# Kernel tuning notes

Measured on AMD Instinct MI355X. Metric: run time of the kernel, lower is better.

## Reference

```python
import jax, jax.numpy as jnp
import numpy as np

EMBED = 512
HEADS = 8
HEAD_DIM = EMBED // HEADS


def setup_inputs() -> dict:
    key = jax.random.key(0)
    ks = jax.random.split(key, 9)
    N, L = 4, 2048
    values = jax.random.normal(ks[0], (N, L, EMBED), dtype=jnp.float32)
    keys = jax.random.normal(ks[1], (N, L, EMBED), dtype=jnp.float32)
    query = jax.random.normal(ks[2], (N, L, EMBED), dtype=jnp.float32)
    mask = jax.random.randint(ks[3], (N, 1, 1, L), 0, 2, dtype=jnp.int32)
    s_h = 1.0 / np.sqrt(HEAD_DIM).astype(np.float32)
    s_e = 1.0 / np.sqrt(EMBED).astype(np.float32)
    Wv = jax.random.normal(ks[4], (HEAD_DIM, HEAD_DIM), dtype=jnp.float32) * s_h
    Wk = jax.random.normal(ks[5], (HEAD_DIM, HEAD_DIM), dtype=jnp.float32) * s_h
    Wq = jax.random.normal(ks[6], (HEAD_DIM, HEAD_DIM), dtype=jnp.float32) * s_h
    Wo = jax.random.normal(ks[7], (EMBED, EMBED), dtype=jnp.float32) * s_e
    bo = jnp.zeros((EMBED,), dtype=jnp.float32)
    return {"values": values, "keys": keys, "query": query, "mask": mask,
            "Wv": Wv, "Wk": Wk, "Wq": Wq, "Wo": Wo, "bo": bo}


def reference(values, keys, query, mask, Wv, Wk, Wq, Wo, bo):
    N, Lq, E = query.shape
    D = Wv.shape[0]
    H = E // D
    Lk = keys.shape[1]
    # split heads: [N, L, H, D]
    v = values.reshape(N, values.shape[1], H, D)
    k = keys.reshape(N, Lk, H, D)
    q = query.reshape(N, Lq, H, D)
    # per-head linear projections (nn.Linear: x @ W^T, no bias)
    v = jnp.einsum("nlhd,ed->nlhe", v, Wv)
    k = jnp.einsum("nlhd,ed->nlhe", k, Wk)
    q = jnp.einsum("nlhd,ed->nlhe", q, Wq)
    # energy: [N, H, Lq, Lk]
    energy = jnp.einsum("nqhd,nkhd->nhqk", q, k)
    energy = jnp.where(mask == 0, jnp.float32(-1e20), energy)
    # NOTE: original scales by sqrt(embed_size), not sqrt(head_dim)
    attn = jax.nn.softmax(energy / jnp.sqrt(jnp.float32(E)), axis=3)
    out = jnp.einsum("nhqk,nkhd->nqhd", attn, v).reshape(N, Lq, E)
    return out @ Wo.T + bo
```

## Files before the change

### kernel.cpp

```cpp
#include <hip/hip_runtime.h>

#define LSEQ 2048
#define EMB  512
#define NH   8
#define HD   64
#define NBATCH 4
#define QSCALE (0.044194173824159216f * 1.4426950408889634f)

using short8  = __attribute__((ext_vector_type(8))) short;
using short4v = __attribute__((ext_vector_type(4))) short;
using f32x4   = __attribute__((ext_vector_type(4))) float;

__device__ __forceinline__ short bf16r(float f) {
  union { float f; unsigned u; } x; x.f = f;
  unsigned r = x.u + 0x7FFFu + ((x.u >> 16) & 1u);
  return (short)(r >> 16);
}

__device__ __forceinline__ float exp2v(float x) {
  float r;
  asm("v_exp_f32 %0, %1" : "=v"(r) : "v"(x));
  return r;
}

__device__ __forceinline__ unsigned cvtpk(float lo, float hi) {
  unsigned r;
  asm("v_cvt_pk_bf16_f32 %0, %1, %2" : "=v"(r) : "v"(lo), "v"(hi));
  return r;
}

__device__ __forceinline__ void stage16(const void* g, void* l) {
  __builtin_amdgcn_global_load_lds(
      (const __attribute__((address_space(1))) unsigned int*)g,
      (__attribute__((address_space(3))) unsigned int*)l, 16, 0, 0);
}

__device__ __forceinline__ short8 cvt8(const float* __restrict__ p) {
  float4 a = ((const float4*)p)[0];
  float4 b = ((const float4*)p)[1];
  short8 r;
  r[0]=bf16r(a.x); r[1]=bf16r(a.y); r[2]=bf16r(a.z); r[3]=bf16r(a.w);
  r[4]=bf16r(b.x); r[5]=bf16r(b.y); r[6]=bf16r(b.z); r[7]=bf16r(b.w);
  return r;
}

__device__ __forceinline__ short8 ld8(const short* __restrict__ p) {
  return *(const short8*)p;
}

__global__ __launch_bounds__(256) void prep_kernel(
    const int* __restrict__ mask, float* __restrict__ fbias,
    int* __restrict__ kidx, int* __restrict__ meta,
    const float* __restrict__ Wq, const float* __restrict__ Wk,
    const float* __restrict__ Wv, short* __restrict__ Wqb,
    short* __restrict__ Wkb, short* __restrict__ Wvb) {
  __shared__ int ssum[256];
  int b = blockIdx.x;
  int tid = threadIdx.x;
  if (b < 4) {
    int n = b;
    int base = n * LSEQ;
    int loc[8], c = 0;
#pragma unroll
    for (int j = 0; j < 8; j++) { loc[j] = mask[base + tid * 8 + j] != 0; c += loc[j]; }
    ssum[tid] = c;
    __syncthreads();
    for (int off = 1; off < 256; off <<= 1) {
      int v = (tid >= off) ? ssum[tid - off] : 0;
      __syncthreads();
      ssum[tid] += v;
      __syncthreads();
    }
    int total = ssum[255];
    int excl = ssum[tid] - c;
    int qz = (total == 0);
#pragma unroll
    for (int j = 0; j < 8; j++) {
      int i = tid * 8 + j;
      kidx[base + i] = qz ? i : 0;
      fbias[base + i] = (qz || i < total) ? 0.f : -1e30f;
    }
    __syncthreads();
    if (!qz) {
      int pos = excl;
#pragma unroll
      for (int j = 0; j < 8; j++)
        if (loc[j]) { kidx[base + pos] = tid * 8 + j; pos++; }
    }
    if (tid == 0) {
      meta[n] = qz ? (LSEQ / 64) : ((total + 63) >> 6);
      meta[4 + n] = qz;
    }
  } else {
    int t = (b - 4) >> 2;
    int i = ((b - 4) & 3) * 256 + tid;
    const float* W = (t == 0) ? Wq : (t == 1) ? Wk : Wv;
    short* O = (t == 0) ? Wqb : (t == 1) ? Wkb : Wvb;
    float sc = (t == 0) ? QSCALE : 1.f;
    float4 v = ((const float4*)W)[i];
    short4v r;
    r[0]=bf16r(v.x*sc); r[1]=bf16r(v.y*sc); r[2]=bf16r(v.z*sc); r[3]=bf16r(v.w*sc);
    ((short4v*)O)[i] = r;
  }
}

__global__ __launch_bounds__(256) void proj_kernel(
    const float* __restrict__ query, const float* __restrict__ keys,
    const float* __restrict__ values,
    const short* __restrict__ Wqb, const short* __restrict__ Wkb,
    const short* __restrict__ Wvb, const int* __restrict__ kidx,
    const int* __restrict__ meta,
    short* __restrict__ Qp, short* __restrict__ Kp, short* __restrict__ Vt) {
  __shared__ short tile[64][72];
  int t = blockIdx.y;
  const float* x = (t == 0) ? query : (t == 1) ? keys : values;
  const short* W = (t == 0) ? Wqb   : (t == 1) ? Wkb  : Wvb;
  int idx = blockIdx.x;
  int lt = idx & 31, h = (idx >> 5) & 7, n = idx >> 8;
  int tid = threadIdx.x, lane = tid & 63, w = tid >> 6;
  int row16 = lane & 15, g = lane >> 4;
  int lbase = lt * 64 + w * 16;

  int zq = 0;
  const float* xr;
  int lrow = lbase + row16;
  if (t == 0) {
    zq = meta[4 + n];
    xr = x + ((size_t)(n * LSEQ + lrow)) * EMB + h * HD + g * 8;
  } else {
    if (lbase >= ((meta[n] + 1) & ~1) * 64) return;
    int gidx = kidx[n * LSEQ + lrow];
    xr = x + ((size_t)(n * LSEQ + gidx)) * EMB + h * HD + g * 8;
  }
  short8 a0 = cvt8(xr);
  short8 a1 = cvt8(xr + 32);

  f32x4 acc[4];
#pragma unroll
  for (int et = 0; et < 4; et++) acc[et] = (f32x4){0.f, 0.f, 0.f, 0.f};
#pragma unroll
  for (int et = 0; et < 4; et++) {
    const short* wr = W + (size_t)(et * 16 + row16) * HD + g * 8;
    short8 b0 = ld8(wr);
    short8 b1 = ld8(wr + 32);
    acc[et] = __builtin_amdgcn_mfma_f32_16x16x32_bf16(a0, b0, acc[et], 0, 0, 0);
    acc[et] = __builtin_amdgcn_mfma_f32_16x16x32_bf16(a1, b1, acc[et], 0, 0, 0);
  }
  if (zq) {
#pragma unroll
    for (int et = 0; et < 4; et++) acc[et] = (f32x4){0.f, 0.f, 0.f, 0.f};
  }

  if (t == 2) {
#pragma unroll
    for (int et = 0; et < 4; et++)
#pragma unroll
      for (int r = 0; r < 4; r++)
        tile[et * 16 + row16][w * 16 + g * 4 + r] = bf16r(acc[et][r]);
  } else {
#pragma unroll
    for (int et = 0; et < 4; et++)
#pragma unroll
      for (int r = 0; r < 4; r++)
        tile[w * 16 + g * 4 + r][et * 16 + row16] = bf16r(acc[et][r]);
  }
  __syncthreads();

  size_t nh = (size_t)(n * NH + h);
#pragma unroll
  for (int i = tid; i < 512; i += 256) {
    int rr = i >> 3, cc = i & 7;
    short8 v = *(const short8*)&tile[rr][cc * 8];
    if (t == 2)
      *(short8*)(Vt + (nh * HD + rr) * LSEQ + lt * 64 + cc * 8) = v;
    else {
      short* O = (t == 0) ? Qp : Kp;
      *(short8*)(O + (nh * LSEQ + lt * 64 + rr) * HD + cc * 8) = v;
    }
  }
}

__global__ __launch_bounds__(512, 1) void attn_kernel(
    const short* __restrict__ Qp, const short* __restrict__ Kp,
    const short* __restrict__ Vt, const float* __restrict__ fbias,
    const int* __restrict__ meta, short* __restrict__ aout,
    const float* __restrict__ Wo, short* __restrict__ Wob) {
  __shared__ __align__(16) char smem[98304];

  int idx = blockIdx.x;
  int tid = threadIdx.x;
  if (idx >= NBATCH * NH * (LSEQ / 256)) {
    int i = (idx - NBATCH * NH * (LSEQ / 256)) * 512 + tid;
    float4 v = ((const float4*)Wo)[i];
    short4v r;
    r[0]=bf16r(v.x); r[1]=bf16r(v.y); r[2]=bf16r(v.z); r[3]=bf16r(v.w);
    ((short4v*)Wob)[i] = r;
    return;
  }
  int h = idx & 7;
  int qt = (idx >> 3) & 7;
  int n = idx >> 6;
  int lane = tid & 63, w = tid >> 6;
  int q0 = lane & 15, g = lane >> 4;
  int xr = q0 & 7;
  int nkt = (meta[n] + 1) >> 1;

  size_t nh = (size_t)(n * NH + h);
  const short* Qb = Qp + (nh * LSEQ + qt * 256 + w * 32) * HD;
  short8 bq00 = ld8(Qb + q0 * HD + g * 8);
  short8 bq01 = ld8(Qb + q0 * HD + 32 + g * 8);
  short8 bq10 = ld8(Qb + (16 + q0) * HD + g * 8);
  short8 bq11 = ld8(Qb + (16 + q0) * HD + 32 + g * 8);

  f32x4 acc0[4], acc1[4];
#pragma unroll
  for (int dt = 0; dt < 4; dt++) {
    acc0[dt] = (f32x4){0.f, 0.f, 0.f, 0.f};
    acc1[dt] = (f32x4){0.f, 0.f, 0.f, 0.f};
  }
  float l0 = 0.f, l1 = 0.f;

  const char* Ksrc = (const char*)(Kp + nh * (size_t)LSEQ * HD);
  const char* Vsrc = (const char*)(Vt + nh * (size_t)HD * LSEQ);
  const float* fb  = fbias + n * LSEQ + g * 4;

  int ksoff[2], vsoff[2], ldo[2];
#pragma unroll
  for (int j = 0; j < 2; j++) {
    int c = j * 512 + w * 64 + lane;
    int rK = c >> 3, cwK = (c & 7) ^ (rK & 7);
    ksoff[j] = rK * 128 + cwK * 16;
    int rV = c >> 4, cwV = c & 15;
    int sub = (cwV & 7) ^ (rV & 7);
    vsoff[j] = rV * (LSEQ * 2) + ((cwV & 8) + sub) * 16;
    ldo[j] = (j * 512 + w * 64) * 16;
  }

  int kfragb = q0 * 128 + ((g ^ xr) << 4);
  int vfragb = q0 * 256 + ((g ^ xr) << 4);
  int pbase = 65536 + w * 4096 + q0 * 128;
  char* pw_[4];
#pragma unroll
  for (int ks = 0; ks < 4; ks++)
    pw_[ks] = smem + pbase + ((ks * 32 + g * 8) ^ (xr << 4));
  const char* pr0 = smem + pbase + ((g * 16) ^ (xr << 4));
  const char* pr1 = smem + pbase + ((64 + g * 16) ^ (xr << 4));

#pragma unroll
  for (int j = 0; j < 2; j++) stage16(Ksrc + ksoff[j], smem + ldo[j]);
#pragma unroll
  for (int j = 0; j < 2; j++) stage16(Vsrc + vsoff[j], smem + 32768 + ldo[j]);
  __syncthreads();

  for (int kt = 0; kt < nkt; kt++) {
    int buf = kt & 1;
    if (kt < nkt - 1) {
      int bo = (buf ^ 1) * 16384;
      const char* Kn = Ksrc + (size_t)(kt + 1) * (128 * 128);
      const char* Vn = Vsrc + (size_t)(kt + 1) * 256;
#pragma unroll
      for (int j = 0; j < 2; j++) stage16(Kn + ksoff[j], smem + bo + ldo[j]);
#pragma unroll
      for (int j = 0; j < 2; j++) stage16(Vn + vsoff[j], smem + 32768 + bo + ldo[j]);
    }

#pragma unroll
    for (int h2 = 0; h2 < 2; h2++) {
      f32x4 fbv[4];
#pragma unroll
      for (int ks = 0; ks < 4; ks++)
        fbv[ks] = *(const f32x4*)(fb + kt * 128 + h2 * 64 + ks * 16);

      int kb_l = buf * 16384 + h2 * 8192 + kfragb;
      f32x4 s0[4], s1[4];
      __builtin_amdgcn_s_setprio(1);
#pragma unroll
      for (int ks = 0; ks < 4; ks++) {
        short8 k0 = *(const short8*)(smem + (kb_l + ks * 2048));
        short8 k1 = *(const short8*)(smem + ((kb_l + ks * 2048) ^ 64));
        f32x4 t0 = __builtin_amdgcn_mfma_f32_16x16x32_bf16(k0, bq00, fbv[ks], 0, 0, 0);
        s0[ks]   = __builtin_amdgcn_mfma_f32_16x16x32_bf16(k1, bq01, t0, 0, 0, 0);
        f32x4 t1 = __builtin_amdgcn_mfma_f32_16x16x32_bf16(k0, bq10, fbv[ks], 0, 0, 0);
        s1[ks]   = __builtin_amdgcn_mfma_f32_16x16x32_bf16(k1, bq11, t1, 0, 0, 0);
      }
      __builtin_amdgcn_s_setprio(0);

      float ps0 = 0.f, ps1 = 0.f;
#pragma unroll
      for (int ks = 0; ks < 4; ks++) {
        float p0 = exp2v(s0[ks][0] - 32.f), p1 = exp2v(s0[ks][1] - 32.f);
        float p2 = exp2v(s0[ks][2] - 32.f), p3 = exp2v(s0[ks][3] - 32.f);
        ps0 += (p0 + p1) + (p2 + p3);
        *(int2*)pw_[ks] = make_int2((int)cvtpk(p0, p1), (int)cvtpk(p2, p3));
        float q1 = exp2v(s1[ks][0] - 32.f), q2 = exp2v(s1[ks][1] - 32.f);
        float q3 = exp2v(s1[ks][2] - 32.f), q4 = exp2v(s1[ks][3] - 32.f);
        ps1 += (q1 + q2) + (q3 + q4);
        *(int2*)(pw_[ks] + 2048) = make_int2((int)cvtpk(q1, q2), (int)cvtpk(q3, q4));
      }
      l0 += ps0; l1 += ps1;

      asm volatile("s_waitcnt lgkmcnt(0)" ::: "memory");

      short8 ap00 = *(const short8*)pr0;
      short8 ap01 = *(const short8*)pr1;
      short8 ap10 = *(const short8*)(pr0 + 2048);
      short8 ap11 = *(const short8*)(pr1 + 2048);
      int vb_l = 32768 + buf * 16384 + vfragb + h2 * 128;
      __builtin_amdgcn_s_setprio(1);
#pragma unroll
      for (int dt = 0; dt < 4; dt++) {
        short8 v0 = *(const short8*)(smem + (vb_l + dt * 4096));
        short8 v1 = *(const short8*)(smem + ((vb_l + dt * 4096) ^ 64));
        acc0[dt] = __builtin_amdgcn_mfma_f32_16x16x32_bf16(ap00, v0, acc0[dt], 0, 0, 0);
        acc0[dt] = __builtin_amdgcn_mfma_f32_16x16x32_bf16(ap01, v1, acc0[dt], 0, 0, 0);
        acc1[dt] = __builtin_amdgcn_mfma_f32_16x16x32_bf16(ap10, v0, acc1[dt], 0, 0, 0);
        acc1[dt] = __builtin_amdgcn_mfma_f32_16x16x32_bf16(ap11, v1, acc1[dt], 0, 0, 0);
      }
      __builtin_amdgcn_s_setprio(0);
    }

    __syncthreads();
  }

  l0 += __shfl_xor(l0, 16);  l0 += __shfl_xor(l0, 32);
  l1 += __shfl_xor(l1, 16);  l1 += __shfl_xor(l1, 32);
  float li0 = l0 > 0.f ? 1.f / l0 : 0.f;
  float li1 = l1 > 0.f ? 1.f / l1 : 0.f;
  int lb = lane & 48;
  float w0[4], w1[4];
#pragma unroll
  for (int r = 0; r < 4; r++) {
    w0[r] = __shfl(li0, lb + g * 4 + r);
    w1[r] = __shfl(li1, lb + g * 4 + r);
  }
  int qrow = qt * 256 + w * 32;
#pragma unroll
  for (int r = 0; r < 4; r++) {
    size_t o0 = ((size_t)(n * LSEQ + qrow + g * 4 + r)) * EMB + h * HD;
    size_t o1 = ((size_t)(n * LSEQ + qrow + 16 + g * 4 + r)) * EMB + h * HD;
#pragma unroll
    for (int dt = 0; dt < 4; dt++) {
      aout[o0 + dt * 16 + q0] = bf16r(acc0[dt][r] * w0[r]);
      aout[o1 + dt * 16 + q0] = bf16r(acc1[dt][r] * w1[r]);
    }
  }
}

__global__ __launch_bounds__(256) void outproj_kernel(
    const short* __restrict__ aout, const short* __restrict__ Wob,
    const float* __restrict__ bo, float* __restrict__ out) {
  int mt = blockIdx.x, nt = blockIdx.y;
  int tid = threadIdx.x, lane = tid & 63, w = tid >> 6;
  int row16 = lane & 15, g = lane >> 4;
  int mrow = mt * 256 + w * 64;

  f32x4 acc[4][4];
#pragma unroll
  for (int hh = 0; hh < 4; hh++)
#pragma unroll
    for (int et = 0; et < 4; et++) acc[hh][et] = (f32x4){0.f, 0.f, 0.f, 0.f};

  for (int kc = 0; kc < 16; kc++) {
    short8 a[4];
#pragma unroll
    for (int hh = 0; hh < 4; hh++)
      a[hh] = ld8(aout + (size_t)(mrow + hh * 16 + row16) * EMB + kc * 32 + g * 8);
#pragma unroll
    for (int et = 0; et < 4; et++) {
      short8 bw = ld8(Wob + (size_t)(nt * 64 + et * 16 + row16) * EMB + kc * 32 + g * 8);
#pragma unroll
      for (int hh = 0; hh < 4; hh++)
        acc[hh][et] = __builtin_amdgcn_mfma_f32_16x16x32_bf16(a[hh], bw, acc[hh][et], 0, 0, 0);
    }
  }
#pragma unroll
  for (int et = 0; et < 4; et++) {
    int e = nt * 64 + et * 16 + row16;
    float bias = bo[e];
#pragma unroll
    for (int hh = 0; hh < 4; hh++)
#pragma unroll
      for (int r = 0; r < 4; r++)
        out[(size_t)(mrow + hh * 16 + g * 4 + r) * EMB + e] = acc[hh][et][r] + bias;
  }
}

extern "C" void kernel_launch(void* const* d_in, const int* in_sizes, int n_in,
                              void* d_out, int out_size, void* d_ws, size_t ws_size,
                              hipStream_t stream) {
  const float* values = (const float*)d_in[0];
  const float* keys   = (const float*)d_in[1];
  const float* query  = (const float*)d_in[2];
  const int*   mask   = (const int*)d_in[3];
  const float* Wv     = (const float*)d_in[4];
  const float* Wk     = (const float*)d_in[5];
  const float* Wq     = (const float*)d_in[6];
  const float* Wo     = (const float*)d_in[7];
  const float* bo     = (const float*)d_in[8];
  float* out = (float*)d_out;

  short* Qp = (short*)d_out;
  short* Kp = (short*)((char*)d_out + (8u << 20));
  char* ws = (char*)d_ws;
  short* Vt    = (short*)(ws);
  short* aout  = (short*)(ws + (8u << 20));
  short* Wob   = (short*)(ws + (16u << 20));
  float* fbias = (float*)(ws + (16u << 20) + (512u << 10));
  int*   kidx  = (int*)  (ws + (16u << 20) + (544u << 10));
  int*   meta  = (int*)  (ws + (16u << 20) + (576u << 10));
  short* Wqb   = (short*)(ws + (16u << 20) + (577u << 10));
  short* Wkb   = (short*)(ws + (16u << 20) + (585u << 10));
  short* Wvb   = (short*)(ws + (16u << 20) + (593u << 10));

  prep_kernel<<<16, 256, 0, stream>>>(mask, fbias, kidx, meta,
                                      Wq, Wk, Wv, Wqb, Wkb, Wvb);
  proj_kernel<<<dim3(NBATCH * NH * (LSEQ / 64), 3), 256, 0, stream>>>(
      query, keys, values, Wqb, Wkb, Wvb, kidx, meta, Qp, Kp, Vt);
  attn_kernel<<<NBATCH * NH * (LSEQ / 256) + 128, 512, 0, stream>>>(
      Qp, Kp, Vt, fbias, meta, aout, Wo, Wob);
  outproj_kernel<<<dim3((NBATCH * LSEQ) / 256, EMB / 64), 256, 0, stream>>>(
      aout, Wob, bo, out);
}
```

Measured before the change: 84.00 us.

## Fuse four kernels into two cooperative launches with grid-wide syncs

Merges prep and projection into one cooperative kernel, and attention and output projection into another, with grid.sync between the phases instead of separate launches. The Wo bf16 conversion moves into the first fused kernel, and the output projection is remapped onto the 256 attention blocks, using 128 of them with 8 waves each. This is meant to cut launch overheads and inter-kernel gaps. The cost is grid-sync overhead, reduced parallelism in the outproj phase (128 blocks instead of 256), and reliance on all 1536 or 256 blocks being co-resident, with a fallback to separate launches if the cooperative launch fails.

After: 299.7 us. 257% more time.

```diff
diff --git a/kernel.cpp b/kernel.cpp
--- a/kernel.cpp
+++ b/kernel.cpp
@@ -1,4 +1,7 @@
 #include <hip/hip_runtime.h>
+#include <hip/hip_cooperative_groups.h>
+
+namespace cg = cooperative_groups;
 
 #define LSEQ 2048
 #define EMB  512
@@ -48,87 +51,69 @@
   return *(const short8*)p;
 }
 
-__global__ __launch_bounds__(256) void prep_kernel(
-    const int* __restrict__ mask, float* __restrict__ fbias,
-    int* __restrict__ kidx, int* __restrict__ meta,
-    const float* __restrict__ Wq, const float* __restrict__ Wk,
-    const float* __restrict__ Wv, short* __restrict__ Wqb,
-    short* __restrict__ Wkb, short* __restrict__ Wvb) {
-  __shared__ int ssum[256];
-  int b = blockIdx.x;
-  int tid = threadIdx.x;
-  if (b < 4) {
-    int n = b;
-    int base = n * LSEQ;
-    int loc[8], c = 0;
-#pragma unroll
-    for (int j = 0; j < 8; j++) { loc[j] = mask[base + tid * 8 + j] != 0; c += loc[j]; }
-    ssum[tid] = c;
+
+__device__ __forceinline__ void compact_phase(int n, const int* __restrict__ mask,
+                                              float* __restrict__ fbias,
+                                              int* __restrict__ kidx,
+                                              int* __restrict__ meta, int* ssum,
+                                              int tid) {
+  int base = n * LSEQ;
+  int loc[8], c = 0;
+#pragma unroll
+  for (int j = 0; j < 8; j++) { loc[j] = mask[base + tid * 8 + j] != 0; c += loc[j]; }
+  ssum[tid] = c;
+  __syncthreads();
+  for (int off = 1; off < 256; off <<= 1) {
+    int v = (tid >= off) ? ssum[tid - off] : 0;
     __syncthreads();
-    for (int off = 1; off < 256; off <<= 1) {
-      int v = (tid >= off) ? ssum[tid - off] : 0;
-      __syncthreads();
-      ssum[tid] += v;
-      __syncthreads();
-    }
-    int total = ssum[255];
-    int excl = ssum[tid] - c;
-    int qz = (total == 0);
-#pragma unroll
-    for (int j = 0; j < 8; j++) {
-      int i = tid * 8 + j;
-      kidx[base + i] = qz ? i : 0;
-      fbias[base + i] = (qz || i < total) ? 0.f : -1e30f;
-    }
+    ssum[tid] += v;
     __syncthreads();
-    if (!qz) {
-      int pos = excl;
-#pragma unroll
-      for (int j = 0; j < 8; j++)
-        if (loc[j]) { kidx[base + pos] = tid * 8 + j; pos++; }
-    }
-    if (tid == 0) {
-      meta[n] = qz ? (LSEQ / 64) : ((total + 63) >> 6);
-      meta[4 + n] = qz;
-    }
-  } else {
-    int t = (b - 4) >> 2;
-    int i = ((b - 4) & 3) * 256 + tid;
-    const float* W = (t == 0) ? Wq : (t == 1) ? Wk : Wv;
-    short* O = (t == 0) ? Wqb : (t == 1) ? Wkb : Wvb;
-    float sc = (t == 0) ? QSCALE : 1.f;
-    float4 v = ((const float4*)W)[i];
-    short4v r;
-    r[0]=bf16r(v.x*sc); r[1]=bf16r(v.y*sc); r[2]=bf16r(v.z*sc); r[3]=bf16r(v.w*sc);
-    ((short4v*)O)[i] = r;
-  }
-}
-
-__global__ __launch_bounds__(256) void proj_kernel(
+  }
+  int total = ssum[255];
+  int excl = ssum[tid] - c;
+  int qz = (total == 0);
+#pragma unroll
+  for (int j = 0; j < 8; j++) {
+    int i = tid * 8 + j;
+    kidx[base + i] = qz ? i : 0;
+    fbias[base + i] = (qz || i < total) ? 0.f : -1e30f;
+  }
+  __syncthreads();
+  if (!qz) {
+    int pos = excl;
+#pragma unroll
+    for (int j = 0; j < 8; j++)
+      if (loc[j]) { kidx[base + pos] = tid * 8 + j; pos++; }
+  }
+  if (tid == 0) {
+    meta[n] = qz ? (LSEQ / 64) : ((total + 63) >> 6);
+    meta[4 + n] = qz;
+  }
+}
+
+__device__ __forceinline__ void proj_unit(
+    int u, int tid, short (*tile)[72],
     const float* __restrict__ query, const float* __restrict__ keys,
     const float* __restrict__ values,
     const short* __restrict__ Wqb, const short* __restrict__ Wkb,
     const short* __restrict__ Wvb, const int* __restrict__ kidx,
     const int* __restrict__ meta,
     short* __restrict__ Qp, short* __restrict__ Kp, short* __restrict__ Vt) {
-  __shared__ short tile[64][72];
-  int t = blockIdx.y;
+  int t = u >> 10, pidx = u & 1023;
+  int lt = pidx & 31, h = (pidx >> 5) & 7, n = pidx >> 8;
+  if (t != 0 && lt * 64 >= ((meta[n] + 1) & ~1) * 64) return;
   const float* x = (t == 0) ? query : (t == 1) ? keys : values;
   const short* W = (t == 0) ? Wqb   : (t == 1) ? Wkb  : Wvb;
-  int idx = blockIdx.x;
-  int lt = idx & 31, h = (idx >> 5) & 7, n = idx >> 8;
-  int tid = threadIdx.x, lane = tid & 63, w = tid >> 6;
+  int lane = tid & 63, w = tid >> 6;
   int row16 = lane & 15, g = lane >> 4;
   int lbase = lt * 64 + w * 16;
-
+  int lrow = lbase + row16;
   int zq = 0;
   const float* xr;
-  int lrow = lbase + row16;
   if (t == 0) {
     zq = meta[4 + n];
     xr = x + ((size_t)(n * LSEQ + lrow)) * EMB + h * HD + g * 8;
   } else {
-    if (lbase >= ((meta[n] + 1) & ~1) * 64) return;
     int gidx = kidx[n * LSEQ + lrow];
     xr = x + ((size_t)(n * LSEQ + gidx)) * EMB + h * HD + g * 8;
   }
@@ -167,7 +152,6 @@
   __syncthreads();
 
   size_t nh = (size_t)(n * NH + h);
-#pragma unroll
   for (int i = tid; i < 512; i += 256) {
     int rr = i >> 3, cc = i & 7;
     short8 v = *(const short8*)&tile[rr][cc * 8];
@@ -180,23 +164,11 @@
   }
 }
 
-__global__ __launch_bounds__(512, 1) void attn_kernel(
+__device__ __forceinline__ void attn_block(
+    int idx, int tid, char* smem,
     const short* __restrict__ Qp, const short* __restrict__ Kp,
     const short* __restrict__ Vt, const float* __restrict__ fbias,
-    const int* __restrict__ meta, short* __restrict__ aout,
-    const float* __restrict__ Wo, short* __restrict__ Wob) {
-  __shared__ __align__(16) char smem[98304];
-
-  int idx = blockIdx.x;
-  int tid = threadIdx.x;
-  if (idx >= NBATCH * NH * (LSEQ / 256)) {
-    int i = (idx - NBATCH * NH * (LSEQ / 256)) * 512 + tid;
-    float4 v = ((const float4*)Wo)[i];
-    short4v r;
-    r[0]=bf16r(v.x); r[1]=bf16r(v.y); r[2]=bf16r(v.z); r[3]=bf16r(v.w);
-    ((short4v*)Wob)[i] = r;
-    return;
-  }
+    const int* __restrict__ meta, short* __restrict__ aout) {
   int h = idx & 7;
   int qt = (idx >> 3) & 7;
   int n = idx >> 6;
@@ -346,43 +318,170 @@
   }
 }
 
+__device__ __forceinline__ void outproj_wave(
+    int mrow, int nt, int lane, const short* __restrict__ aout,
+    const short* __restrict__ Wob, const float* __restrict__ bo,
+    float* __restrict__ out) {
+  int row16 = lane & 15, g = lane >> 4;
+  f32x4 acc[4][4];
+#pragma unroll
+  for (int hh = 0; hh < 4; hh++)
+#pragma unroll
+    for (int et = 0; et < 4; et++) acc[hh][et] = (f32x4){0.f, 0.f, 0.f, 0.f};
+
+  for (int kc = 0; kc < 16; kc++) {
+    short8 a[4];
+#pragma unroll
+    for (int hh = 0; hh < 4; hh++)
+      a[hh] = ld8(aout + (size_t)(mrow + hh * 16 + row16) * EMB + kc * 32 + g * 8);
+#pragma unroll
+    for (int et = 0; et < 4; et++) {
+      short8 bw = ld8(Wob + (size_t)(nt * 64 + et * 16 + row16) * EMB + kc * 32 + g * 8);
+#pragma unroll
+      for (int hh = 0; hh < 4; hh++)
+        acc[hh][et] = __builtin_amdgcn_mfma_f32_16x16x32_bf16(a[hh], bw, acc[hh][et], 0, 0, 0);
+    }
+  }
+#pragma unroll
+  for (int et = 0; et < 4; et++) {
+    int e = nt * 64 + et * 16 + row16;
+    float bias = bo[e];
+#pragma unroll
+    for (int hh = 0; hh < 4; hh++)
+#pragma unroll
+      for (int r = 0; r < 4; r++)
+        out[(size_t)(mrow + hh * 16 + g * 4 + r) * EMB + e] = acc[hh][et][r] + bias;
+  }
+}
+
+__global__ __launch_bounds__(256, 6) void fusedA(
+    const int* __restrict__ mask, float* __restrict__ fbias,
+    int* __restrict__ kidx, int* __restrict__ meta,
+    const float* __restrict__ Wq, const float* __restrict__ Wk,
+    const float* __restrict__ Wv, const float* __restrict__ Wo,
+    short* __restrict__ Wqb, short* __restrict__ Wkb, short* __restrict__ Wvb,
+    short* __restrict__ Wob,
+    const float* __restrict__ query, const float* __restrict__ keys,
+    const float* __restrict__ values,
+    short* __restrict__ Qp, short* __restrict__ Kp, short* __restrict__ Vt) {
+  __shared__ __align__(16) char smA[9216];
+  int b = blockIdx.x, tid = threadIdx.x;
+
+  if (b < 4) {
+    compact_phase(b, mask, fbias, kidx, meta, (int*)smA, tid);
+  } else if (b < 16) {
+    int t = (b - 4) >> 2;
+    int i = ((b - 4) & 3) * 256 + tid;
+    const float* W = (t == 0) ? Wq : (t == 1) ? Wk : Wv;
+    short* O = (t == 0) ? Wqb : (t == 1) ? Wkb : Wvb;
+    float sc = (t == 0) ? QSCALE : 1.f;
+    float4 v = ((const float4*)W)[i];
+    short4v r;
+    r[0]=bf16r(v.x*sc); r[1]=bf16r(v.y*sc); r[2]=bf16r(v.z*sc); r[3]=bf16r(v.w*sc);
+    ((short4v*)O)[i] = r;
+  } else if (b < 272) {
+    int i = (b - 16) * 256 + tid;
+    float4 v = ((const float4*)Wo)[i];
+    short4v r;
+    r[0]=bf16r(v.x); r[1]=bf16r(v.y); r[2]=bf16r(v.z); r[3]=bf16r(v.w);
+    ((short4v*)Wob)[i] = r;
+  }
+  cg::this_grid().sync();
+
+  short (*tile)[72] = (short(*)[72])smA;
+#pragma unroll
+  for (int it = 0; it < 2; it++) {
+    int u = b + it * 1536;
+    proj_unit(u, tid, tile, query, keys, values, Wqb, Wkb, Wvb, kidx, meta,
+              Qp, Kp, Vt);
+    __syncthreads();
+  }
+}
+
+__global__ __launch_bounds__(512, 1) void fusedB(
+    const short* __restrict__ Qp, const short* __restrict__ Kp,
+    const short* __restrict__ Vt, const float* __restrict__ fbias,
+    const int* __restrict__ meta, short* __restrict__ aout,
+    const short* __restrict__ Wob, const float* __restrict__ bo,
+    float* __restrict__ out) {
+  __shared__ __align__(16) char smem[98304];
+  int b = blockIdx.x, tid = threadIdx.x;
+
+  attn_block(b, tid, smem, Qp, Kp, Vt, fbias, meta, aout);
+  cg::this_grid().sync();
+
+  if (b < 128) {
+    int lane = tid & 63, w8 = tid >> 6;
+    int mt = b >> 2, ntp = b & 3;
+    int mrow = mt * 256 + (w8 & 3) * 64;
+    int nt = ntp * 2 + (w8 >> 2);
+    outproj_wave(mrow, nt, lane, aout, Wob, bo, out);
+  }
+}
+
+
+__global__ __launch_bounds__(256) void prep_kernel(
+    const int* __restrict__ mask, float* __restrict__ fbias,
+    int* __restrict__ kidx, int* __restrict__ meta,
+    const float* __restrict__ Wq, const float* __restrict__ Wk,
+    const float* __restrict__ Wv, short* __restrict__ Wqb,
+    short* __restrict__ Wkb, short* __restrict__ Wvb) {
+  __shared__ int ssum[256];
+  int b = blockIdx.x;
+  int tid = threadIdx.x;
+  if (b < 4) {
+    compact_phase(b, mask, fbias, kidx, meta, ssum, tid);
+  } else {
+    int t = (b - 4) >> 2;
+    int i = ((b - 4) & 3) * 256 + tid;
+    const float* W = (t == 0) ? Wq : (t == 1) ? Wk : Wv;
+    short* O = (t == 0) ? Wqb : (t == 1) ? Wkb : Wvb;
+    float sc = (t == 0) ? QSCALE : 1.f;
+    float4 v = ((const float4*)W)[i];
+    short4v r;
+    r[0]=bf16r(v.x*sc); r[1]=bf16r(v.y*sc); r[2]=bf16r(v.z*sc); r[3]=bf16r(v.w*sc);
+    ((short4v*)O)[i] = r;
+  }
+}
+
+__global__ __launch_bounds__(256) void proj_kernel(
+    const float* __restrict__ query, const float* __restrict__ keys,
+    const float* __restrict__ values,
+    const short* __restrict__ Wqb, const short* __restrict__ Wkb,
+    const short* __restrict__ Wvb, const int* __restrict__ kidx,
+    const int* __restrict__ meta,
+    short* __restrict__ Qp, short* __restrict__ Kp, short* __restrict__ Vt) {
+  __shared__ short tile[64][72];
+  int u = blockIdx.y * 1024 + blockIdx.x;
+  proj_unit(u, threadIdx.x, tile, query, keys, values, Wqb, Wkb, Wvb,
+            kidx, meta, Qp, Kp, Vt);
+}
+
+__global__ __launch_bounds__(512, 1) void attn_kernel(
+    const short* __restrict__ Qp, const short* __restrict__ Kp,
+    const short* __restrict__ Vt, const float* __restrict__ fbias,
+    const int* __restrict__ meta, short* __restrict__ aout,
+    const float* __restrict__ Wo, short* __restrict__ Wob) {
+  __shared__ __align__(16) char smem[98304];
+  int idx = blockIdx.x;
+  int tid = threadIdx.x;
+  if (idx >= NBATCH * NH * (LSEQ / 256)) {
+    int i = (idx - NBATCH * NH * (LSEQ / 256)) * 512 + tid;
+    float4 v = ((const float4*)Wo)[i];
+    short4v r;
+    r[0]=bf16r(v.x); r[1]=bf16r(v.y); r[2]=bf16r(v.z); r[3]=bf16r(v.w);
+    ((short4v*)Wob)[i] = r;
+    return;
+  }
+  attn_block(idx, tid, smem, Qp, Kp, Vt, fbias, meta, aout);
+}
+
 __global__ __launch_bounds__(256) void outproj_kernel(
     const short* __restrict__ aout, const short* __restrict__ Wob,
     const float* __restrict__ bo, float* __restrict__ out) {
-  int mt = blockIdx.x, nt = blockIdx.y;
-  int tid = threadIdx.x, lane = tid & 63, w = tid >> 6;
-  int row16 = lane & 15, g = lane >> 4;
-  int mrow = mt * 256 + w * 64;
-
-  f32x4 acc[4][4];
-#pragma unroll
-  for (int hh = 0; hh < 4; hh++)
-#pragma unroll
-    for (int et = 0; et < 4; et++) acc[hh][et] = (f32x4){0.f, 0.f, 0.f, 0.f};
-
-  for (int kc = 0; kc < 16; kc++) {
-    short8 a[4];
-#pragma unroll
-    for (int hh = 0; hh < 4; hh++)
-      a[hh] = ld8(aout + (size_t)(mrow + hh * 16 + row16) * EMB + kc * 32 + g * 8);
-#pragma unroll
-    for (int et = 0; et < 4; et++) {
-      short8 bw = ld8(Wob + (size_t)(nt * 64 + et * 16 + row16) * EMB + kc * 32 + g * 8);
-#pragma unroll
-      for (int hh = 0; hh < 4; hh++)
-        acc[hh][et] = __builtin_amdgcn_mfma_f32_16x16x32_bf16(a[hh], bw, acc[hh][et], 0, 0, 0);
-    }
-  }
-#pragma unroll
-  for (int et = 0; et < 4; et++) {
-    int e = nt * 64 + et * 16 + row16;
-    float bias = bo[e];
-#pragma unroll
-    for (int hh = 0; hh < 4; hh++)
-#pragma unroll
-      for (int r = 0; r < 4; r++)
-        out[(size_t)(mrow + hh * 16 + g * 4 + r) * EMB + e] = acc[hh][et][r] + bias;
-  }
+  int lane = threadIdx.x & 63, w = threadIdx.x >> 6;
+  int mrow = blockIdx.x * 256 + w * 64;
+  outproj_wave(mrow, blockIdx.y, lane, aout, Wob, bo, out);
 }
 
 extern "C" void kernel_launch(void* const* d_in, const int* in_sizes, int n_in,
@@ -412,12 +511,37 @@
   short* Wkb   = (short*)(ws + (16u << 20) + (585u << 10));
   short* Wvb   = (short*)(ws + (16u << 20) + (593u << 10));
 
-  prep_kernel<<<16, 256, 0, stream>>>(mask, fbias, kidx, meta,
-                                      Wq, Wk, Wv, Wqb, Wkb, Wvb);
-  proj_kernel<<<dim3(NBATCH * NH * (LSEQ / 64), 3), 256, 0, stream>>>(
-      query, keys, values, Wqb, Wkb, Wvb, kidx, meta, Qp, Kp, Vt);
-  attn_kernel<<<NBATCH * NH * (LSEQ / 256) + 128, 512, 0, stream>>>(
-      Qp, Kp, Vt, fbias, meta, aout, Wo, Wob);
-  outproj_kernel<<<dim3((NBATCH * LSEQ) / 256, EMB / 64), 256, 0, stream>>>(
-      aout, Wob, bo, out);
-}
+  void* argsA[] = {
+      (void*)&mask, (void*)&fbias, (void*)&kidx, (void*)&meta,
+      (void*)&Wq, (void*)&Wk, (void*)&Wv, (void*)&Wo,
+      (void*)&Wqb, (void*)&Wkb, (void*)&Wvb, (void*)&Wob,
+      (void*)&query, (void*)&keys, (void*)&values,
+      (void*)&Qp, (void*)&Kp, (void*)&Vt};
+  void* argsB[] = {
+      (void*)&Qp, (void*)&Kp, (void*)&Vt, (void*)&fbias, (void*)&meta,
+      (void*)&aout, (void*)&Wob, (void*)&bo, (void*)&out};
+
+  hipError_t ea = hipLaunchCooperativeKernel(
+      (const void*)fusedA, dim3(1536), dim3(256), argsA, 0, stream);
+  if (ea == hipSuccess) {
+    hipError_t eb = hipLaunchCooperativeKernel(
+        (const void*)fusedB, dim3(256), dim3(512), argsB, 0, stream);
+    if (eb != hipSuccess) {
+      (void)hipGetLastError();
+      attn_kernel<<<NBATCH * NH * (LSEQ / 256) + 128, 512, 0, stream>>>(
+          Qp, Kp, Vt, fbias, meta, aout, Wo, Wob);
+      outproj_kernel<<<dim3((NBATCH * LSEQ) / 256, EMB / 64), 256, 0, stream>>>(
+          aout, Wob, bo, out);
+    }
+  } else {
+    (void)hipGetLastError();
+    prep_kernel<<<16, 256, 0, stream>>>(mask, fbias, kidx, meta,
+                                        Wq, Wk, Wv, Wqb, Wkb, Wvb);
+    proj_kernel<<<dim3(1024, 3), 256, 0, stream>>>(
+        query, keys, values, Wqb, Wkb, Wvb, kidx, meta, Qp, Kp, Vt);
+    attn_kernel<<<NBATCH * NH * (LSEQ / 256) + 128, 512, 0, stream>>>(
+        Qp, Kp, Vt, fbias, meta, aout, Wo, Wob);
+    outproj_kernel<<<dim3((NBATCH * LSEQ) / 256, EMB / 64), 256, 0, stream>>>(
+        aout, Wob, bo, out);
+  }
+}
```

## Fuse Q projection into attention kernel prologue via LDS staging

Applied to the files above, without the earlier changes.

Moves the per-head query projection out of the separate projection kernel and into the attention kernel's prologue. Each wave loads its fp32 query rows, multiplies them with the bf16 Wq fragments using MFMA, and writes the result in swizzled form to its P-tile region of shared memory, where it is read back as the Q operands. This removes writing Qp to global memory and reading it back, and shrinks the projection grid to K and V only. In exchange, attention blocks read fp32 query data at the start of the kernel, which lengthens the prologue, and correctness relies on the transposed MFMA operand order matching the expected layout.

Result: faster. 78.77 us (-6.2%).

```diff
diff --git a/kernel.cpp b/kernel.cpp
--- a/kernel.cpp
+++ b/kernel.cpp
@@ -105,33 +105,23 @@
 }
 
 __global__ __launch_bounds__(256) void proj_kernel(
-    const float* __restrict__ query, const float* __restrict__ keys,
-    const float* __restrict__ values,
-    const short* __restrict__ Wqb, const short* __restrict__ Wkb,
-    const short* __restrict__ Wvb, const int* __restrict__ kidx,
-    const int* __restrict__ meta,
-    short* __restrict__ Qp, short* __restrict__ Kp, short* __restrict__ Vt) {
+    const float* __restrict__ keys, const float* __restrict__ values,
+    const short* __restrict__ Wkb, const short* __restrict__ Wvb,
+    const int* __restrict__ kidx, const int* __restrict__ meta,
+    short* __restrict__ Kp, short* __restrict__ Vt) {
   __shared__ short tile[64][72];
-  int t = blockIdx.y;
-  const float* x = (t == 0) ? query : (t == 1) ? keys : values;
-  const short* W = (t == 0) ? Wqb   : (t == 1) ? Wkb  : Wvb;
+  int t = blockIdx.y + 1;
+  const float* x = (t == 1) ? keys : values;
+  const short* W = (t == 1) ? Wkb  : Wvb;
   int idx = blockIdx.x;
   int lt = idx & 31, h = (idx >> 5) & 7, n = idx >> 8;
   int tid = threadIdx.x, lane = tid & 63, w = tid >> 6;
   int row16 = lane & 15, g = lane >> 4;
   int lbase = lt * 64 + w * 16;
 
-  int zq = 0;
-  const float* xr;
-  int lrow = lbase + row16;
-  if (t == 0) {
-    zq = meta[4 + n];
-    xr = x + ((size_t)(n * LSEQ + lrow)) * EMB + h * HD + g * 8;
-  } else {
-    if (lbase >= ((meta[n] + 1) & ~1) * 64) return;
-    int gidx = kidx[n * LSEQ + lrow];
-    xr = x + ((size_t)(n * LSEQ + gidx)) * EMB + h * HD + g * 8;
-  }
+  if (lbase >= ((meta[n] + 1) & ~1) * 64) return;
+  int gidx = kidx[n * LSEQ + lbase + row16];
+  const float* xr = x + ((size_t)(n * LSEQ + gidx)) * EMB + h * HD + g * 8;
   short8 a0 = cvt8(xr);
   short8 a1 = cvt8(xr + 32);
 
@@ -146,10 +136,6 @@
     acc[et] = __builtin_amdgcn_mfma_f32_16x16x32_bf16(a0, b0, acc[et], 0, 0, 0);
     acc[et] = __builtin_amdgcn_mfma_f32_16x16x32_bf16(a1, b1, acc[et], 0, 0, 0);
   }
-  if (zq) {
-#pragma unroll
-    for (int et = 0; et < 4; et++) acc[et] = (f32x4){0.f, 0.f, 0.f, 0.f};
-  }
 
   if (t == 2) {
 #pragma unroll
@@ -173,18 +159,17 @@
     short8 v = *(const short8*)&tile[rr][cc * 8];
     if (t == 2)
       *(short8*)(Vt + (nh * HD + rr) * LSEQ + lt * 64 + cc * 8) = v;
-    else {
-      short* O = (t == 0) ? Qp : Kp;
-      *(short8*)(O + (nh * LSEQ + lt * 64 + rr) * HD + cc * 8) = v;
-    }
+    else
+      *(short8*)(Kp + (nh * LSEQ + lt * 64 + rr) * HD + cc * 8) = v;
   }
 }
 
 __global__ __launch_bounds__(512, 1) void attn_kernel(
-    const short* __restrict__ Qp, const short* __restrict__ Kp,
-    const short* __restrict__ Vt, const float* __restrict__ fbias,
-    const int* __restrict__ meta, short* __restrict__ aout,
-    const float* __restrict__ Wo, short* __restrict__ Wob) {
+    const float* __restrict__ query, const short* __restrict__ Wqb,
+    const short* __restrict__ Kp, const short* __restrict__ Vt,
+    const float* __restrict__ fbias, const int* __restrict__ meta,
+    short* __restrict__ aout, const float* __restrict__ Wo,
+    short* __restrict__ Wob) {
   __shared__ __align__(16) char smem[98304];
 
   int idx = blockIdx.x;
@@ -206,19 +191,6 @@
   int nkt = (meta[n] + 1) >> 1;
 
   size_t nh = (size_t)(n * NH + h);
-  const short* Qb = Qp + (nh * LSEQ + qt * 256 + w * 32) * HD;
-  short8 bq00 = ld8(Qb + q0 * HD + g * 8);
-  short8 bq01 = ld8(Qb + q0 * HD + 32 + g * 8);
-  short8 bq10 = ld8(Qb + (16 + q0) * HD + g * 8);
-  short8 bq11 = ld8(Qb + (16 + q0) * HD + 32 + g * 8);
-
-  f32x4 acc0[4], acc1[4];
-#pragma unroll
-  for (int dt = 0; dt < 4; dt++) {
-    acc0[dt] = (f32x4){0.f, 0.f, 0.f, 0.f};
-    acc1[dt] = (f32x4){0.f, 0.f, 0.f, 0.f};
-  }
-  float l0 = 0.f, l1 = 0.f;
 
   const char* Ksrc = (const char*)(Kp + nh * (size_t)LSEQ * HD);
   const char* Vsrc = (const char*)(Vt + nh * (size_t)HD * LSEQ);
@@ -250,6 +222,47 @@
   for (int j = 0; j < 2; j++) stage16(Ksrc + ksoff[j], smem + ldo[j]);
 #pragma unroll
   for (int j = 0; j < 2; j++) stage16(Vsrc + vsoff[j], smem + 32768 + ldo[j]);
+
+  {
+    short8 wf0[4], wf1[4];
+#pragma unroll
+    for (int et = 0; et < 4; et++) {
+      wf0[et] = ld8(Wqb + (et * 16 + q0) * HD + g * 8);
+      wf1[et] = ld8(Wqb + (et * 16 + q0) * HD + 32 + g * 8);
+    }
+    int zq = meta[4 + n];
+#pragma unroll
+    for (int hh = 0; hh < 2; hh++) {
+      const float* xrow = query +
+          ((size_t)(n * LSEQ + qt * 256 + w * 32 + hh * 16 + q0)) * EMB +
+          h * HD + g * 8;
+      short8 xa0 = cvt8(xrow);
+      short8 xa1 = cvt8(xrow + 32);
+#pragma unroll
+      for (int et = 0; et < 4; et++) {
+        f32x4 tq = (f32x4){0.f, 0.f, 0.f, 0.f};
+        tq = __builtin_amdgcn_mfma_f32_16x16x32_bf16(wf0[et], xa0, tq, 0, 0, 0);
+        tq = __builtin_amdgcn_mfma_f32_16x16x32_bf16(wf1[et], xa1, tq, 0, 0, 0);
+        if (zq) tq = (f32x4){0.f, 0.f, 0.f, 0.f};
+        *(int2*)(smem + pbase + hh * 2048 + ((et * 32 + g * 8) ^ (xr << 4))) =
+            make_int2((int)cvtpk(tq[0], tq[1]), (int)cvtpk(tq[2], tq[3]));
+      }
+    }
+  }
+  asm volatile("s_waitcnt lgkmcnt(0)" ::: "memory");
+  short8 bq00 = *(const short8*)pr0;
+  short8 bq01 = *(const short8*)pr1;
+  short8 bq10 = *(const short8*)(pr0 + 2048);
+  short8 bq11 = *(const short8*)(pr1 + 2048);
+
+  f32x4 acc0[4], acc1[4];
+#pragma unroll
+  for (int dt = 0; dt < 4; dt++) {
+    acc0[dt] = (f32x4){0.f, 0.f, 0.f, 0.f};
+    acc1[dt] = (f32x4){0.f, 0.f, 0.f, 0.f};
+  }
+  float l0 = 0.f, l1 = 0.f;
+
   __syncthreads();
 
   for (int kt = 0; kt < nkt; kt++) {
@@ -399,8 +412,7 @@
   const float* bo     = (const float*)d_in[8];
   float* out = (float*)d_out;
 
-  short* Qp = (short*)d_out;
-  short* Kp = (short*)((char*)d_out + (8u << 20));
+  short* Kp = (short*)d_out;
   char* ws = (char*)d_ws;
   short* Vt    = (short*)(ws);
   short* aout  = (short*)(ws + (8u << 20));
@@ -414,10 +426,10 @@
 
   prep_kernel<<<16, 256, 0, stream>>>(mask, fbias, kidx, meta,
                                       Wq, Wk, Wv, Wqb, Wkb, Wvb);
-  proj_kernel<<<dim3(NBATCH * NH * (LSEQ / 64), 3), 256, 0, stream>>>(
-      query, keys, values, Wqb, Wkb, Wvb, kidx, meta, Qp, Kp, Vt);
+  proj_kernel<<<dim3(NBATCH * NH * (LSEQ / 64), 2), 256, 0, stream>>>(
+      keys, values, Wkb, Wvb, kidx, meta, Kp, Vt);
   attn_kernel<<<NBATCH * NH * (LSEQ / 256) + 128, 512, 0, stream>>>(
-      Qp, Kp, Vt, fbias, meta, aout, Wo, Wob);
+      query, Wqb, Kp, Vt, fbias, meta, aout, Wo, Wob);
   outproj_kernel<<<dim3((NBATCH * LSEQ) / 256, EMB / 64), 256, 0, stream>>>(
       aout, Wob, bo, out);
 }
```
